# Optimization experiments

Measured on AMD Instinct MI355X. Metric: run time of the kernel, lower is better.

The kernel has to match this reference:

```python
import jax, jax.numpy as jnp
import numpy as np

B, D, HGT, WID = 32, 512, 8, 32   # batch, channels, feature map H, W
T = HGT * WID                     # 256 spatial tokens
NH, L, MAXLEN = 8, 2, 25          # heads, encoder layers, max text len


def _ln(x, s, b, eps=1e-5):
    m = jnp.mean(x, -1, keepdims=True)
    v = jnp.mean((x - m) ** 2, -1, keepdims=True)
    return (x - m) * jax.lax.rsqrt(v + eps) * s + b


def setup_inputs() -> dict:
    key = jax.random.key(0)
    ks = jax.random.split(key, 16)
    w = lambda k, shp: jax.random.normal(k, shp, jnp.float32) * 0.02
    return {
        "x": jax.random.normal(ks[0], (B, D, HGT, WID), jnp.float32),
        "encoder_word_pos": jnp.arange(T, dtype=jnp.int32),
        "gsrm_word_pos": jnp.arange(MAXLEN, dtype=jnp.int32),
        # encoder positional table
        "pos_table": w(ks[1], (T, D)),
        # per-layer encoder params (stacked over L)
        "ln1_s": jnp.ones((L, D), jnp.float32), "ln1_b": jnp.zeros((L, D), jnp.float32),
        "Wq": w(ks[2], (L, D, D)), "bq": jnp.zeros((L, D), jnp.float32),
        "Wk": w(ks[3], (L, D, D)), "bk": jnp.zeros((L, D), jnp.float32),
        "Wv": w(ks[4], (L, D, D)), "bv": jnp.zeros((L, D), jnp.float32),
        "Wo": w(ks[5], (L, D, D)), "bo": jnp.zeros((L, D), jnp.float32),
        "ln2_s": jnp.ones((L, D), jnp.float32), "ln2_b": jnp.zeros((L, D), jnp.float32),
        "W1": w(ks[6], (L, D, D)), "b1": jnp.zeros((L, D), jnp.float32),  # d_inner_hid = hidden_dim
        "W2": w(ks[7], (L, D, D)), "b2": jnp.zeros((L, D), jnp.float32),
        "lnf_s": jnp.ones((D,), jnp.float32), "lnf_b": jnp.zeros((D,), jnp.float32),
        # PVAM head params
        "fc0_w": w(ks[8], (D, D)), "fc0_b": jnp.zeros((D,), jnp.float32),
        "emb_table": w(ks[9], (MAXLEN, D)),
        "fc1_w": w(ks[10], (D,)),
    }


def _pvam(x, encoder_word_pos, gsrm_word_pos, pos_table,
          ln1_s, ln1_b, Wq, bq, Wk, bk, Wv, bv, Wo, bo,
          ln2_s, ln2_b, W1, b1, W2, b2, lnf_s, lnf_b,
          fc0_w, fc0_b, emb_table, fc1_w):
    b, c, h, wd = x.shape
    feat = x.reshape(b, c, h * wd).transpose(0, 2, 1)          # [b, t, c]
    # prepare encoder: scale + learned positional embedding (eval mode: no dropout)
    enc = feat * jnp.sqrt(jnp.float32(c)) + pos_table[encoder_word_pos]
    dk = c // NH
    scale = 1.0 / jnp.sqrt(jnp.float32(dk))
    for l in range(L):  # pre-norm transformer encoder (preprocess='n', postprocess='da')
        qin = _ln(enc, ln1_s[l], ln1_b[l])
        q = (qin @ Wq[l] + bq[l]).reshape(b, -1, NH, dk)
        k = (qin @ Wk[l] + bk[l]).reshape(b, -1, NH, dk)
        v = (qin @ Wv[l] + bv[l]).reshape(b, -1, NH, dk)
        p = jax.nn.softmax(jnp.einsum('bqhd,bkhd->bhqk', q, k) * scale, -1)
        o = jnp.einsum('bhqk,bkhd->bqhd', p, v).reshape(b, -1, c)
        enc = enc + (o @ Wo[l] + bo[l])
        y = _ln(enc, ln2_s[l], ln2_b[l])
        enc = enc + (jax.nn.relu(y @ W1[l] + b1[l]) @ W2[l] + b2[l])
    enc = _ln(enc, lnf_s, lnf_b)
    word_features = enc @ fc0_w + fc0_b                        # [b, t, c]
    word_pos = emb_table[gsrm_word_pos]                        # [max_len, c]
    # additive attention: tanh(broadcast add) -> scalar score -> softmax over t
    y = jnp.tanh(word_features[:, None, :, :] + word_pos[None, :, None, :])  # [b,max_len,t,c]
    attn = jax.nn.softmax(jnp.einsum('bmtc,c->bmt', y, fc1_w), -1)
    return jnp.einsum('bmt,btc->bmc', attn, word_features)    # [b, max_len, c]


def reference(x, encoder_word_pos, gsrm_word_pos, pos_table,
              ln1_s, ln1_b, Wq, bq, Wk, bk, Wv, bv, Wo, bo,
              ln2_s, ln2_b, W1, b1, W2, b2, lnf_s, lnf_b,
              fc0_w, fc0_b, emb_table, fc1_w):
    return _pvam(x, encoder_word_pos, gsrm_word_pos, pos_table,
                 ln1_s, ln1_b, Wq, bq, Wk, bk, Wv, bv, Wo, bo,
                 ln2_s, ln2_b, W1, b1, W2, b2, lnf_s, lnf_b,
                 fc0_w, fc0_b, emb_table, fc1_w)
```

## Files before the change

### kernel.cpp

```cpp
#include <hip/hip_runtime.h>
#include <math.h>

#define B_ 32
#define D_ 512
#define T_ 256
#define NH_ 8
#define DK_ 64
#define ML_ 25

typedef unsigned short ushort_t;
using short8 = __attribute__((ext_vector_type(8))) short;
using f32x4  = __attribute__((ext_vector_type(4))) float;

__device__ __forceinline__ ushort_t f2bf(float f) {
    unsigned u = __float_as_uint(f);
    unsigned r = (u + 0x7fffu + ((u >> 16) & 1u)) >> 16;
    return (ushort_t)r;
}
__device__ __forceinline__ float bf2f(ushort_t h) {
    return __uint_as_float(((unsigned)h) << 16);
}
__device__ __forceinline__ void gl16(const void* g, void* l) {
    __builtin_amdgcn_global_load_lds((const __attribute__((address_space(1))) void*)g,
                                     (__attribute__((address_space(3))) void*)l, 16, 0, 0);
}
#define ZERO4(v) { (v)[0]=0.f; (v)[1]=0.f; (v)[2]=0.f; (v)[3]=0.f; }

__global__ __launch_bounds__(256) void prep_kernel(const float* __restrict__ x,
                                                   const int* __restrict__ epos,
                                                   const float* __restrict__ pos,
                                                   float* __restrict__ enc) {
    __shared__ float ld[64][65];
    int tt = blockIdx.x, ct = blockIdx.y, b = blockIdx.z;
    int t0 = tt * 64, c0 = ct * 64;
    int tid = threadIdx.x;
    int r = tid >> 4, c4 = (tid & 15) << 2;
#pragma unroll
    for (int p = 0; p < 4; p++) {
        int row = p * 16 + r;
        float4 v = *(const float4*)(x + ((size_t)(b * D_ + c0 + row) * T_ + t0) + c4);
        ld[row][c4 + 0] = v.x; ld[row][c4 + 1] = v.y; ld[row][c4 + 2] = v.z; ld[row][c4 + 3] = v.w;
    }
    __syncthreads();
#pragma unroll
    for (int p = 0; p < 4; p++) {
        int tr = p * 16 + r;
        int ep = epos[t0 + tr];
        float4 pv = *(const float4*)(pos + (size_t)ep * D_ + c0 + c4);
        float4 o;
        o.x = ld[c4 + 0][tr] * 22.627417f + pv.x;
        o.y = ld[c4 + 1][tr] * 22.627417f + pv.y;
        o.z = ld[c4 + 2][tr] * 22.627417f + pv.z;
        o.w = ld[c4 + 3][tr] * 22.627417f + pv.w;
        *(float4*)(enc + (size_t)(b * T_ + t0 + tr) * D_ + c0 + c4) = o;
    }
}

__global__ __launch_bounds__(256) void convert_w_kernel(const float* __restrict__ Wq,
                                                        const float* __restrict__ Wk,
                                                        const float* __restrict__ Wv,
                                                        const float* __restrict__ Wo,
                                                        const float* __restrict__ W1,
                                                        const float* __restrict__ W2,
                                                        const float* __restrict__ fc0,
                                                        ushort_t* __restrict__ wt) {
    __shared__ float ld[64][65];
    int m = blockIdx.x >> 6;
    int tile = blockIdx.x & 63;
    int tn = tile >> 3, tk = tile & 7;
    int n0 = tn * 64, k0 = tk * 64;
    const float* src;
    if (m < 12) {
        int l = m / 6, w = m % 6;
        const float* bases[6] = {Wq, Wk, Wv, Wo, W1, W2};
        src = bases[w] + (size_t)l * D_ * D_;
    } else {
        src = fc0;
    }
    int tid = threadIdx.x;
    int r = tid >> 4, c4 = (tid & 15) << 2;
#pragma unroll
    for (int p = 0; p < 4; p++) {
        int row = p * 16 + r;
        float4 v = *(const float4*)(src + (size_t)(k0 + row) * D_ + n0 + c4);
        ld[row][c4 + 0] = v.x; ld[row][c4 + 1] = v.y; ld[row][c4 + 2] = v.z; ld[row][c4 + 3] = v.w;
    }
    __syncthreads();
    ushort_t* dsth = wt + (size_t)m * D_ * D_;
    ushort_t* dstl = wt + (size_t)13 * D_ * D_;
#pragma unroll
    for (int p = 0; p < 4; p++) {
        int n = p * 16 + r;
        int kc = c4;
        ushort_t h[4], lo[4];
#pragma unroll
        for (int i = 0; i < 4; i++) {
            float f = ld[kc + i][n];
            h[i] = f2bf(f);
            lo[i] = f2bf(f - bf2f(h[i]));
        }
        *(ushort4*)(dsth + (size_t)(n0 + n) * D_ + k0 + kc) = make_ushort4(h[0], h[1], h[2], h[3]);
        if (m == 12)
            *(ushort4*)(dstl + (size_t)(n0 + n) * D_ + k0 + kc) = make_ushort4(lo[0], lo[1], lo[2], lo[3]);
    }
}

template<bool LO>
__global__ __launch_bounds__(256) void ln_kernel(const float* __restrict__ x,
                                                 const float* __restrict__ s,
                                                 const float* __restrict__ b,
                                                 ushort_t* __restrict__ yh,
                                                 ushort_t* __restrict__ yl) {
    int wid = threadIdx.x >> 6, lane = threadIdx.x & 63;
    size_t row = (size_t)blockIdx.x * 4 + wid;
    const float4* xr = (const float4*)(x + row * D_);
    float4 v0 = xr[lane * 2], v1 = xr[lane * 2 + 1];
    float sum = v0.x + v0.y + v0.z + v0.w + v1.x + v1.y + v1.z + v1.w;
    for (int o = 32; o; o >>= 1) sum += __shfl_xor(sum, o);
    float mean = sum * (1.f / 512.f);
    float d[8] = {v0.x - mean, v0.y - mean, v0.z - mean, v0.w - mean,
                  v1.x - mean, v1.y - mean, v1.z - mean, v1.w - mean};
    float vs = 0.f;
#pragma unroll
    for (int i = 0; i < 8; i++) vs += d[i] * d[i];
    for (int o = 32; o; o >>= 1) vs += __shfl_xor(vs, o);
    float rs = 1.f / sqrtf(vs * (1.f / 512.f) + 1e-5f);
    const float4* s4 = (const float4*)s;
    const float4* b4 = (const float4*)b;
    float4 sa = s4[lane * 2], sb = s4[lane * 2 + 1];
    float4 ba = b4[lane * 2], bb = b4[lane * 2 + 1];
    float o8[8];
    o8[0] = d[0] * rs * sa.x + ba.x; o8[1] = d[1] * rs * sa.y + ba.y;
    o8[2] = d[2] * rs * sa.z + ba.z; o8[3] = d[3] * rs * sa.w + ba.w;
    o8[4] = d[4] * rs * sb.x + bb.x; o8[5] = d[5] * rs * sb.y + bb.y;
    o8[6] = d[6] * rs * sb.z + bb.z; o8[7] = d[7] * rs * sb.w + bb.w;
    ushort_t h[8];
#pragma unroll
    for (int i = 0; i < 8; i++) h[i] = f2bf(o8[i]);
    uint4 u;
    u.x = (unsigned)h[0] | ((unsigned)h[1] << 16);
    u.y = (unsigned)h[2] | ((unsigned)h[3] << 16);
    u.z = (unsigned)h[4] | ((unsigned)h[5] << 16);
    u.w = (unsigned)h[6] | ((unsigned)h[7] << 16);
    *(uint4*)(yh + row * D_ + lane * 8) = u;
    if (LO) {
        ushort_t l8[8];
#pragma unroll
        for (int i = 0; i < 8; i++) l8[i] = f2bf(o8[i] - bf2f(h[i]));
        uint4 ul;
        ul.x = (unsigned)l8[0] | ((unsigned)l8[1] << 16);
        ul.y = (unsigned)l8[2] | ((unsigned)l8[3] << 16);
        ul.z = (unsigned)l8[4] | ((unsigned)l8[5] << 16);
        ul.w = (unsigned)l8[6] | ((unsigned)l8[7] << 16);
        *(uint4*)(yl + row * D_ + lane * 8) = ul;
    }
}

template<int EPI>
__global__ __launch_bounds__(256) void gemm_kernel(const ushort_t* __restrict__ A0,
                                                   const ushort_t* __restrict__ A1,
                                                   const ushort_t* __restrict__ A2,
                                                   const ushort_t* __restrict__ B0,
                                                   const ushort_t* __restrict__ B1,
                                                   const ushort_t* __restrict__ B2,
                                                   int nseg, int nbn,
                                                   const float* __restrict__ bias,
                                                   const float* __restrict__ res,
                                                   float* __restrict__ outF,
                                                   ushort_t* __restrict__ outB) {
    __shared__ ushort_t As[3][128 * 64];
    __shared__ ushort_t Bs[3][64 * 64];
    int tid = threadIdx.x;
    int g = blockIdx.x;
    int per = gridDim.x >> 3;
    int lin = (g & 7) * per + (g >> 3);
    int bm = lin / nbn, bn = lin % nbn;

    int lane = tid & 63;
    int wid = tid >> 6;
    int wm = wid >> 1, wn = wid & 1;
    int xr = (lane & 7) << 3;

    f32x4 acc[4][2];
#pragma unroll
    for (int i = 0; i < 4; i++)
#pragma unroll
        for (int j = 0; j < 2; j++) ZERO4(acc[i][j]);

    int nt = nseg * 8;

#define STAGE(kt, buf)                                                                  \
    {                                                                                   \
        int seg_ = (kt) >> 3;                                                           \
        int k0_ = ((kt) & 7) * 64;                                                      \
        const ushort_t* Asg = seg_ == 0 ? A0 : (seg_ == 1 ? A1 : A2);                   \
        const ushort_t* Bsg = seg_ == 0 ? B0 : (seg_ == 1 ? B1 : B2);                   \
        _Pragma("unroll")                                                               \
        for (int it = 0; it < 4; it++) {                                                \
            int uu = tid + it * 256;                                                    \
            int row_ = uu >> 3;                                                         \
            int kb_ = (((uu & 7) ^ (row_ & 7)) << 3);                                   \
            gl16(Asg + (size_t)(bm * 128 + row_) * 512 + k0_ + kb_, &As[buf][uu * 8]);  \
        }                                                                               \
        _Pragma("unroll")                                                               \
        for (int it = 0; it < 2; it++) {                                                \
            int uu = tid + it * 256;                                                    \
            int row_ = uu >> 3;                                                         \
            int kb_ = (((uu & 7) ^ (row_ & 7)) << 3);                                   \
            gl16(Bsg + (size_t)(bn * 64 + row_) * 512 + k0_ + kb_, &Bs[buf][uu * 8]);   \
        }                                                                               \
    }

#define COMPUTE(bufc)                                                                        \
    {                                                                                        \
        _Pragma("unroll")                                                                    \
        for (int kc = 0; kc < 2; kc++) {                                                     \
            short8 a[4], b[2];                                                               \
            int koff = (kc * 32 + ((lane >> 4) << 3)) ^ xr;                                  \
            _Pragma("unroll")                                                                \
            for (int i = 0; i < 4; i++)                                                      \
                a[i] = *(const short8*)&As[bufc][(wm * 64 + i * 16 + (lane & 15)) * 64 + koff]; \
            _Pragma("unroll")                                                                \
            for (int j = 0; j < 2; j++)                                                      \
                b[j] = *(const short8*)&Bs[bufc][(wn * 32 + j * 16 + (lane & 15)) * 64 + koff]; \
            _Pragma("unroll")                                                                \
            for (int i = 0; i < 4; i++)                                                      \
                _Pragma("unroll")                                                            \
                for (int j = 0; j < 2; j++)                                                  \
                    acc[i][j] = __builtin_amdgcn_mfma_f32_16x16x32_bf16(a[i], b[j], acc[i][j], 0, 0, 0); \
        }                                                                                    \
    }

    STAGE(0, 0);
    if (nt > 1) STAGE(1, 1);
    asm volatile("s_waitcnt vmcnt(6)" ::: "memory");
    __builtin_amdgcn_s_barrier();

    int cur = 0;
    for (int t = 0; t < nt; t++) {
        if (t + 2 < nt) STAGE(t + 2, (cur + 2 >= 3 ? cur - 1 : cur + 2));
        COMPUTE(cur);
        if (t + 2 < nt) {
            asm volatile("s_waitcnt vmcnt(6)" ::: "memory");
        } else if (t + 1 < nt) {
            asm volatile("s_waitcnt vmcnt(0)" ::: "memory");
        }
        __builtin_amdgcn_s_barrier();
        cur = (cur == 2) ? 0 : cur + 1;
    }
#undef STAGE
#undef COMPUTE

#pragma unroll
    for (int i = 0; i < 4; i++) {
#pragma unroll
        for (int j = 0; j < 2; j++) {
            int r0 = bm * 128 + wm * 64 + i * 16 + ((lane >> 4) << 2);
            int col = bn * 64 + wn * 32 + j * 16 + (lane & 15);
            float bc = bias[col];
#pragma unroll
            for (int jj = 0; jj < 4; jj++) {
                float v = acc[i][j][jj] + bc;
                int row = r0 + jj;
                size_t idx = (size_t)row * 512 + col;
                if (EPI == 2) {
                    outF[idx] = v + res[idx];
                } else if (EPI == 3) {
                    outB[idx] = f2bf(fmaxf(v, 0.f));
                } else {
                    outF[idx] = v;
                }
            }
        }
    }
}

__global__ __launch_bounds__(256) void gemm_qkv_kernel(const ushort_t* __restrict__ A,
                                                       const ushort_t* __restrict__ W,
                                                       const float* __restrict__ bq,
                                                       const float* __restrict__ bk,
                                                       const float* __restrict__ bv,
                                                       ushort_t* __restrict__ outB) {
    __shared__ ushort_t As[2][128 * 64];
    __shared__ ushort_t Bs[2][128 * 64];
    int tid = threadIdx.x;
    int g = blockIdx.x;
    int per = gridDim.x >> 3;
    int lin = (g & 7) * per + (g >> 3);
    int bm = lin / 12, bn = lin % 12;

    int lane = tid & 63;
    int wid = tid >> 6;
    int wm = wid >> 1, wn = wid & 1;
    int xr = (lane & 7) << 3;

    f32x4 acc[4][4];
#pragma unroll
    for (int i = 0; i < 4; i++)
#pragma unroll
        for (int j = 0; j < 4; j++) ZERO4(acc[i][j]);

#define QSTAGE(kt, buf)                                                                 \
    {                                                                                   \
        int k0_ = (kt) * 64;                                                            \
        _Pragma("unroll")                                                               \
        for (int it = 0; it < 4; it++) {                                                \
            int uu = tid + it * 256;                                                    \
            int row_ = uu >> 3;                                                         \
            int kb_ = (((uu & 7) ^ (row_ & 7)) << 3);                                   \
            gl16(A + (size_t)(bm * 128 + row_) * 512 + k0_ + kb_, &As[buf][uu * 8]);    \
            gl16(W + (size_t)(bn * 128 + row_) * 512 + k0_ + kb_, &Bs[buf][uu * 8]);    \
        }                                                                               \
    }

    QSTAGE(0, 0);
    asm volatile("s_waitcnt vmcnt(0)" ::: "memory");
    __builtin_amdgcn_s_barrier();

    int buf = 0;
    for (int t = 0; t < 8; t++) {
        if (t + 1 < 8) QSTAGE(t + 1, buf ^ 1);
#pragma unroll
        for (int kc = 0; kc < 2; kc++) {
            short8 a[4], b[4];
            int koff = (kc * 32 + ((lane >> 4) << 3)) ^ xr;
#pragma unroll
            for (int i = 0; i < 4; i++)
                a[i] = *(const short8*)&As[buf][(wm * 64 + i * 16 + (lane & 15)) * 64 + koff];
#pragma unroll
            for (int j = 0; j < 4; j++)
                b[j] = *(const short8*)&Bs[buf][(wn * 64 + j * 16 + (lane & 15)) * 64 + koff];
#pragma unroll
            for (int i = 0; i < 4; i++)
#pragma unroll
                for (int j = 0; j < 4; j++)
                    acc[i][j] = __builtin_amdgcn_mfma_f32_16x16x32_bf16(a[i], b[j], acc[i][j], 0, 0, 0);
        }
        if (t + 1 < 8) asm volatile("s_waitcnt vmcnt(0)" ::: "memory");
        __builtin_amdgcn_s_barrier();
        buf ^= 1;
    }
#undef QSTAGE

#pragma unroll
    for (int i = 0; i < 4; i++) {
#pragma unroll
        for (int j = 0; j < 4; j++) {
            int r0 = bm * 128 + wm * 64 + i * 16 + ((lane >> 4) << 2);
            int col = bn * 128 + wn * 64 + j * 16 + (lane & 15);
            int seg = col >> 9;
            int ccol = col & 511;
            const float* bp = (seg == 0) ? bq : (seg == 1 ? bk : bv);
            float bc = bp[ccol];
#pragma unroll
            for (int jj = 0; jj < 4; jj++) {
                float v = acc[i][j][jj] + bc;
                int row = r0 + jj;
                if (seg < 2) {
                    outB[(size_t)seg * 4194304 + (size_t)row * 512 + ccol] = f2bf(v);
                } else {
                    int bb2 = row >> 8, t2 = row & 255;
                    outB[(size_t)2 * 4194304 +
                         ((size_t)(bb2 * 8 + (ccol >> 6)) * 64 + (ccol & 63)) * 256 + t2] = f2bf(v);
                }
            }
        }
    }
}

__global__ __launch_bounds__(256) void attn_fused_kernel(const ushort_t* __restrict__ q,
                                                         const ushort_t* __restrict__ k,
                                                         const ushort_t* __restrict__ vt,
                                                         ushort_t* __restrict__ ao) {
    __shared__ ushort_t KVs[256 * 64];
    __shared__ ushort_t Ps[64 * 256];
    int tid = threadIdx.x;
    int lane = tid & 63;
    int wid = tid >> 6;
    int m0 = blockIdx.x * 64;
    int bh = blockIdx.y;
    int b = bh >> 3, h = bh & 7;
    int xr = (lane & 7) << 3;

#pragma unroll
    for (int it = 0; it < 8; it++) {
        int uu = tid + it * 256;
        int row = uu >> 3;
        int gx = ((uu & 7) ^ (row & 7)) << 3;
        gl16(k + (size_t)(b * T_ + row) * D_ + h * DK_ + gx, &KVs[uu * 8]);
    }
    short8 qa0, qa1;
    {
        int qrow = m0 + wid * 16 + (lane & 15);
        const ushort_t* qp = q + (size_t)(b * T_ + qrow) * D_ + h * DK_ + ((lane >> 4) << 3);
        qa0 = *(const short8*)(qp);
        qa1 = *(const short8*)(qp + 32);
    }
    f32x4 acc[16];
#pragma unroll
    for (int j = 0; j < 16; j++) ZERO4(acc[j]);
    asm volatile("s_waitcnt vmcnt(0)" ::: "memory");
    __syncthreads();

#pragma unroll
    for (int j = 0; j < 16; j++) {
        int krow = j * 16 + (lane & 15);
        short8 b0 = *(const short8*)&KVs[krow * 64 + ((((lane >> 4) << 3)) ^ xr)];
        short8 b1 = *(const short8*)&KVs[krow * 64 + ((32 + ((lane >> 4) << 3)) ^ xr)];
        acc[j] = __builtin_amdgcn_mfma_f32_16x16x32_bf16(qa0, b0, acc[j], 0, 0, 0);
        acc[j] = __builtin_amdgcn_mfma_f32_16x16x32_bf16(qa1, b1, acc[j], 0, 0, 0);
    }
    __syncthreads();

#pragma unroll
    for (int it = 0; it < 8; it++) {
        int uu = tid + it * 256;
        int row = uu >> 5;
        int gx = ((uu & 31) ^ (row & 7)) << 3;
        gl16(vt + ((size_t)bh * DK_ + row) * T_ + gx, &KVs[uu * 8]);
    }

    const float C = 0.125f * 1.44269504f;
#pragma unroll
    for (int jj = 0; jj < 4; jj++) {
        float mx = -1e30f;
#pragma unroll
        for (int j = 0; j < 16; j++) mx = fmaxf(mx, acc[j][jj]);
#pragma unroll
        for (int msk = 1; msk < 16; msk <<= 1) mx = fmaxf(mx, __shfl_xor(mx, msk));
        float sm = 0.f;
#pragma unroll
        for (int j = 0; j < 16; j++) {
            float e = __builtin_amdgcn_exp2f((acc[j][jj] - mx) * C);
            acc[j][jj] = e;
            sm += e;
        }
#pragma unroll
        for (int msk = 1; msk < 16; msk <<= 1) sm += __shfl_xor(sm, msk);
        float inv = 1.f / sm;
#pragma unroll
        for (int j = 0; j < 16; j++) acc[j][jj] *= inv;
    }
#pragma unroll
    for (int j = 0; j < 16; j++) {
#pragma unroll
        for (int jj = 0; jj < 4; jj++) {
            int row = wid * 16 + ((lane >> 4) << 2) + jj;
            int col = j * 16 + (lane & 15);
            Ps[row * 256 + (col ^ ((row & 7) << 3))] = f2bf(acc[j][jj]);
        }
    }
    asm volatile("s_waitcnt vmcnt(0)" ::: "memory");
    __syncthreads();

    int wm = wid >> 1, wn = wid & 1;
    f32x4 acc2[2][2];
#pragma unroll
    for (int i = 0; i < 2; i++)
#pragma unroll
        for (int j = 0; j < 2; j++) ZERO4(acc2[i][j]);
#pragma unroll
    for (int kc = 0; kc < 8; kc++) {
        int off = (kc * 32 + ((lane >> 4) << 3)) ^ xr;
        short8 a0 = *(const short8*)&Ps[(wm * 32 + (lane & 15)) * 256 + off];
        short8 a1 = *(const short8*)&Ps[(wm * 32 + 16 + (lane & 15)) * 256 + off];
        short8 b0 = *(const short8*)&KVs[(wn * 32 + (lane & 15)) * 256 + off];
        short8 b1 = *(const short8*)&KVs[(wn * 32 + 16 + (lane & 15)) * 256 + off];
        acc2[0][0] = __builtin_amdgcn_mfma_f32_16x16x32_bf16(a0, b0, acc2[0][0], 0, 0, 0);
        acc2[0][1] = __builtin_amdgcn_mfma_f32_16x16x32_bf16(a0, b1, acc2[0][1], 0, 0, 0);
        acc2[1][0] = __builtin_amdgcn_mfma_f32_16x16x32_bf16(a1, b0, acc2[1][0], 0, 0, 0);
        acc2[1][1] = __builtin_amdgcn_mfma_f32_16x16x32_bf16(a1, b1, acc2[1][1], 0, 0, 0);
    }
#pragma unroll
    for (int i = 0; i < 2; i++)
#pragma unroll
        for (int j = 0; j < 2; j++)
#pragma unroll
            for (int jj = 0; jj < 4; jj++)
                ao[(size_t)(b * T_ + m0 + wm * 32 + i * 16 + ((lane >> 4) << 2) + jj) * D_ +
                   h * DK_ + wn * 32 + j * 16 + (lane & 15)] = f2bf(acc2[i][j][jj]);
}

__global__ __launch_bounds__(256) void scores_kernel(const float* __restrict__ wf,
                                                     const int* __restrict__ gpos,
                                                     const float* __restrict__ emb,
                                                     const float* __restrict__ w1,
                                                     float* __restrict__ scores) {
    __shared__ float wpL[5][512];
    __shared__ float w1m2[512];
    const float K2 = 2.885390082f;
    int tid = threadIdx.x;
    int b = blockIdx.y;
    int mg = blockIdx.z * 5;
    int t = blockIdx.x * 32 + (tid >> 3);
    int cg = tid & 7;
    for (int idx = tid; idx < 5 * 128; idx += 256) {
        int m = idx >> 7, w4 = idx & 127;
        float4 v = *(const float4*)(emb + (size_t)gpos[mg + m] * D_ + (w4 << 2));
        v.x *= K2; v.y *= K2; v.z *= K2; v.w *= K2;
        *(float4*)&wpL[m][w4 << 2] = v;
    }
    if (tid < 128) {
        float4 v = *(const float4*)(w1 + (tid << 2));
        v.x *= -2.f; v.y *= -2.f; v.z *= -2.f; v.w *= -2.f;
        *(float4*)&w1m2[tid << 2] = v;
    }
    float4 wfs[16];
    float W1S = 0.f;
    const float* wfr = wf + (size_t)(b * T_ + t) * D_ + (cg << 2);
#pragma unroll
    for (int j = 0; j < 16; j++) {
        float4 v = *(const float4*)(wfr + (j << 5));
        wfs[j].x = v.x * K2; wfs[j].y = v.y * K2; wfs[j].z = v.z * K2; wfs[j].w = v.w * K2;
        float4 wv = *(const float4*)(w1 + (cg << 2) + (j << 5));
        W1S += wv.x + wv.y + wv.z + wv.w;
    }
    __syncthreads();
    float s[5] = {W1S, W1S, W1S, W1S, W1S};
#pragma unroll
    for (int j = 0; j < 16; j++) {
        float4 w14 = *(const float4*)&w1m2[(cg << 2) + (j << 5)];
#pragma unroll
        for (int m = 0; m < 5; m++) {
            float4 wp4 = *(const float4*)&wpL[m][(cg << 2) + (j << 5)];
            s[m] += w14.x * __builtin_amdgcn_rcpf(__builtin_amdgcn_exp2f(wfs[j].x + wp4.x) + 1.f);
            s[m] += w14.y * __builtin_amdgcn_rcpf(__builtin_amdgcn_exp2f(wfs[j].y + wp4.y) + 1.f);
            s[m] += w14.z * __builtin_amdgcn_rcpf(__builtin_amdgcn_exp2f(wfs[j].z + wp4.z) + 1.f);
            s[m] += w14.w * __builtin_amdgcn_rcpf(__builtin_amdgcn_exp2f(wfs[j].w + wp4.w) + 1.f);
        }
    }
#pragma unroll
    for (int m = 0; m < 5; m++) {
        s[m] += __shfl_xor(s[m], 1);
        s[m] += __shfl_xor(s[m], 2);
        s[m] += __shfl_xor(s[m], 4);
    }
    if (cg == 0) {
#pragma unroll
        for (int m = 0; m < 5; m++)
            scores[((size_t)b * ML_ + mg + m) * T_ + t] = s[m];
    }
}

__global__ __launch_bounds__(256) void wsum_kernel(const float* __restrict__ scores,
                                                   const float* __restrict__ wf,
                                                   float* __restrict__ out) {
    __shared__ float at[T_][8];
    __shared__ float redmax[4][8];
    __shared__ float redsum[4][8];
    int tid = threadIdx.x;
    int lane = tid & 63, wv = tid >> 6;
    int b = blockIdx.y, m0 = blockIdx.x * 5;
    float s[5];
#pragma unroll
    for (int q = 0; q < 5; q++)
        s[q] = scores[((size_t)b * ML_ + m0 + q) * T_ + tid];
#pragma unroll
    for (int q = 0; q < 5; q++) {
        float mx = s[q];
        for (int o = 32; o; o >>= 1) mx = fmaxf(mx, __shfl_xor(mx, o));
        if (lane == 0) redmax[wv][q] = mx;
    }
    __syncthreads();
    float e[5];
#pragma unroll
    for (int q = 0; q < 5; q++) {
        float m = fmaxf(fmaxf(redmax[0][q], redmax[1][q]), fmaxf(redmax[2][q], redmax[3][q]));
        e[q] = __expf(s[q] - m);
        float sm = e[q];
        for (int o = 32; o; o >>= 1) sm += __shfl_xor(sm, o);
        if (lane == 0) redsum[wv][q] = sm;
    }
    __syncthreads();
#pragma unroll
    for (int q = 0; q < 5; q++) {
        float sm = redsum[0][q] + redsum[1][q] + redsum[2][q] + redsum[3][q];
        at[tid][q] = e[q] / sm;
    }
    __syncthreads();
    int c0 = tid << 1;
    const float* wfb = wf + (size_t)b * T_ * D_ + c0;
    float acc[5][2] = {};
    for (int t = 0; t < T_; t++) {
        float2 v = *(const float2*)(wfb + (size_t)t * D_);
        float4 a4 = *(const float4*)&at[t][0];
        float a5 = at[t][4];
        acc[0][0] += a4.x * v.x; acc[0][1] += a4.x * v.y;
        acc[1][0] += a4.y * v.x; acc[1][1] += a4.y * v.y;
        acc[2][0] += a4.z * v.x; acc[2][1] += a4.z * v.y;
        acc[3][0] += a4.w * v.x; acc[3][1] += a4.w * v.y;
        acc[4][0] += a5 * v.x;   acc[4][1] += a5 * v.y;
    }
#pragma unroll
    for (int q = 0; q < 5; q++) {
        float2 o;
        o.x = acc[q][0]; o.y = acc[q][1];
        *(float2*)(out + ((size_t)b * ML_ + m0 + q) * D_ + c0) = o;
    }
}

extern "C" void kernel_launch(void* const* d_in, const int* in_sizes, int n_in,
                              void* d_out, int out_size, void* d_ws, size_t ws_size,
                              hipStream_t stream) {
    (void)in_sizes; (void)n_in; (void)out_size; (void)ws_size;
    const float* x        = (const float*)d_in[0];
    const int*   epos     = (const int*)d_in[1];
    const int*   gpos     = (const int*)d_in[2];
    const float* pos_tab  = (const float*)d_in[3];
    const float* ln1_s    = (const float*)d_in[4];
    const float* ln1_b    = (const float*)d_in[5];
    const float* Wq       = (const float*)d_in[6];
    const float* bq       = (const float*)d_in[7];
    const float* Wk       = (const float*)d_in[8];
    const float* bk       = (const float*)d_in[9];
    const float* Wv       = (const float*)d_in[10];
    const float* bv       = (const float*)d_in[11];
    const float* Wo       = (const float*)d_in[12];
    const float* bo       = (const float*)d_in[13];
    const float* ln2_s    = (const float*)d_in[14];
    const float* ln2_b    = (const float*)d_in[15];
    const float* W1       = (const float*)d_in[16];
    const float* b1       = (const float*)d_in[17];
    const float* W2       = (const float*)d_in[18];
    const float* b2       = (const float*)d_in[19];
    const float* lnf_s    = (const float*)d_in[20];
    const float* lnf_b    = (const float*)d_in[21];
    const float* fc0_w    = (const float*)d_in[22];
    const float* fc0_b    = (const float*)d_in[23];
    const float* emb      = (const float*)d_in[24];
    const float* fc1_w    = (const float*)d_in[25];

    char* ws = (char*)d_ws;
    float*    enc = (float*)(ws);
    ushort_t* hi  = (ushort_t*)(ws + 16777216);
    ushort_t* qb  = (ushort_t*)(ws + 25165824);
    ushort_t* kb  = (ushort_t*)(ws + 33554432);
    ushort_t* lo  = (ushort_t*)(ws + 33554432);
    float*    scb = (float*)(ws + 33554432);
    ushort_t* vt  = (ushort_t*)(ws + 41943040);
    ushort_t* h1  = (ushort_t*)(ws + 41943040);
    ushort_t* ao  = (ushort_t*)(ws + 50331648);
    float*    wf  = (float*)(ws + 58720256);
    ushort_t* wt  = (ushort_t*)(ws + 75497472);
    const size_t WSL = (size_t)D_ * D_;

    convert_w_kernel<<<13 * 64, 256, 0, stream>>>(Wq, Wk, Wv, Wo, W1, W2, fc0_w, wt);
    prep_kernel<<<dim3(4, 8, 32), 256, 0, stream>>>(x, epos, pos_tab, enc);

    for (int l = 0; l < 2; l++) {
        size_t o1 = (size_t)l * D_;
        const ushort_t* WqkvT = wt + (l * 6 + 0) * WSL;
        const ushort_t* WoT = wt + (l * 6 + 3) * WSL;
        const ushort_t* W1T = wt + (l * 6 + 4) * WSL;
        const ushort_t* W2T = wt + (l * 6 + 5) * WSL;

        ln_kernel<false><<<2048, 256, 0, stream>>>(enc, ln1_s + o1, ln1_b + o1, hi, nullptr);
        gemm_qkv_kernel<<<768, 256, 0, stream>>>(hi, WqkvT, bq + o1, bk + o1, bv + o1, qb);
        attn_fused_kernel<<<dim3(4, 256), 256, 0, stream>>>(qb, kb, vt, ao);
        gemm_kernel<2><<<512, 256, 0, stream>>>(ao, nullptr, nullptr, WoT, nullptr, nullptr,
                                                1, 8, bo + o1, enc, enc, nullptr);
        ln_kernel<false><<<2048, 256, 0, stream>>>(enc, ln2_s + o1, ln2_b + o1, hi, nullptr);
        gemm_kernel<3><<<512, 256, 0, stream>>>(hi, nullptr, nullptr, W1T, nullptr, nullptr,
                                                1, 8, b1 + o1, nullptr, nullptr, h1);
        gemm_kernel<2><<<512, 256, 0, stream>>>(h1, nullptr, nullptr, W2T, nullptr, nullptr,
                                                1, 8, b2 + o1, enc, enc, nullptr);
    }

    ln_kernel<true><<<2048, 256, 0, stream>>>(enc, lnf_s, lnf_b, hi, lo);
    gemm_kernel<4><<<512, 256, 0, stream>>>(hi, lo, hi, wt + 12 * WSL, wt + 12 * WSL, wt + 13 * WSL,
                                            3, 8, fc0_b, nullptr, wf, nullptr);
    scores_kernel<<<dim3(8, 32, 5), 256, 0, stream>>>(wf, gpos, emb, fc1_w, scb);
    wsum_kernel<<<dim3(5, 32), 256, 0, stream>>>(scb, wf, (float*)d_out);
}
```

Before: 295.0 us.

## Fold LayerNorm into GEMM epilogues via row stats and precomputed weight sums

Removes the standalone LayerNorm kernels. Producers (prep and residual GEMMs) now emit bf16 copies of the raw residual and atomically accumulate per-row sum and sum-of-squares. The LN scale is folded into the weights, and per-column u=sum(s*W) and v=sum(b*W) are precomputed, so consumer GEMMs apply mean/rstd normalization in their epilogue. It also drops the third split segment of the final fc0 GEMM. The risks are E[x^2]-mu^2 variance cancellation, precision loss from running the GEMM on unnormalized bf16 activations, and extra atomics plus zero/uv kernels.

```diff
diff --git a/kernel.cpp b/kernel.cpp
--- a/kernel.cpp
+++ b/kernel.cpp
@@ -26,10 +26,62 @@
 }
 #define ZERO4(v) { (v)[0]=0.f; (v)[1]=0.f; (v)[2]=0.f; (v)[3]=0.f; }
 
+#define STATS_F (5 * 8192 * 2)
+#define UV_F    4608
+
+__global__ __launch_bounds__(256) void zero_kernel(float* __restrict__ z) {
+    int idx = blockIdx.x * 256 + threadIdx.x;
+    if (idx < (STATS_F + 2 * UV_F + 3) / 4) {
+        float4 zz = {0.f, 0.f, 0.f, 0.f};
+        ((float4*)z)[idx] = zz;
+    }
+}
+
+__global__ __launch_bounds__(256) void uv_kernel(const float* __restrict__ Wq,
+                                                 const float* __restrict__ Wk,
+                                                 const float* __restrict__ Wv,
+                                                 const float* __restrict__ W1,
+                                                 const float* __restrict__ fc0,
+                                                 const float* __restrict__ ln1_s, const float* __restrict__ ln1_b,
+                                                 const float* __restrict__ ln2_s, const float* __restrict__ ln2_b,
+                                                 const float* __restrict__ lnf_s, const float* __restrict__ lnf_b,
+                                                 float* __restrict__ u, float* __restrict__ v) {
+    int idx = blockIdx.x;
+    int k0 = blockIdx.y * 128;
+    const float* W; const float* s; const float* b; int off;
+    if (idx < 6) {
+        int l = idx / 3, w = idx % 3;
+        W = (w == 0 ? Wq : (w == 1 ? Wk : Wv)) + (size_t)l * D_ * D_;
+        s = ln1_s + l * D_; b = ln1_b + l * D_;
+        off = l * 1536 + w * 512;
+    } else if (idx < 8) {
+        int l = idx - 6;
+        W = W1 + (size_t)l * D_ * D_;
+        s = ln2_s + l * D_; b = ln2_b + l * D_;
+        off = 3072 + l * 512;
+    } else {
+        W = fc0; s = lnf_s; b = lnf_b; off = 4096;
+    }
+    int tid = threadIdx.x;
+#pragma unroll
+    for (int pass = 0; pass < 2; pass++) {
+        int c = tid + pass * 256;
+        float ua = 0.f, va = 0.f;
+        for (int k = k0; k < k0 + 128; k++) {
+            float w = W[(size_t)k * D_ + c];
+            ua += s[k] * w; va += b[k] * w;
+        }
+        atomicAdd(&u[off + c], ua);
+        atomicAdd(&v[off + c], va);
+    }
+}
+
 __global__ __launch_bounds__(256) void prep_kernel(const float* __restrict__ x,
                                                    const int* __restrict__ epos,
                                                    const float* __restrict__ pos,
-                                                   float* __restrict__ enc) {
+                                                   float* __restrict__ enc,
+                                                   ushort_t* __restrict__ hi,
+                                                   float* __restrict__ st) {
     __shared__ float ld[64][65];
     int tt = blockIdx.x, ct = blockIdx.y, b = blockIdx.z;
     int t0 = tt * 64, c0 = ct * 64;
@@ -52,7 +104,19 @@
         o.y = ld[c4 + 1][tr] * 22.627417f + pv.y;
         o.z = ld[c4 + 2][tr] * 22.627417f + pv.z;
         o.w = ld[c4 + 3][tr] * 22.627417f + pv.w;
-        *(float4*)(enc + (size_t)(b * T_ + t0 + tr) * D_ + c0 + c4) = o;
+        size_t row = (size_t)(b * T_ + t0 + tr);
+        *(float4*)(enc + row * D_ + c0 + c4) = o;
+        *(ushort4*)(hi + row * D_ + c0 + c4) = make_ushort4(f2bf(o.x), f2bf(o.y), f2bf(o.z), f2bf(o.w));
+        float sx = o.x + o.y + o.z + o.w;
+        float sq = o.x*o.x + o.y*o.y + o.z*o.z + o.w*o.w;
+        sx += __shfl_xor(sx, 1); sq += __shfl_xor(sq, 1);
+        sx += __shfl_xor(sx, 2); sq += __shfl_xor(sq, 2);
+        sx += __shfl_xor(sx, 4); sq += __shfl_xor(sq, 4);
+        sx += __shfl_xor(sx, 8); sq += __shfl_xor(sq, 8);
+        if ((tid & 15) == 0) {
+            atomicAdd(&st[2 * row], sx);
+            atomicAdd(&st[2 * row + 1], sq);
+        }
     }
 }
 
@@ -63,6 +127,9 @@
                                                         const float* __restrict__ W1,
                                                         const float* __restrict__ W2,
                                                         const float* __restrict__ fc0,
+                                                        const float* __restrict__ ln1_s,
+                                                        const float* __restrict__ ln2_s,
+                                                        const float* __restrict__ lnf_s,
                                                         ushort_t* __restrict__ wt) {
     __shared__ float ld[64][65];
     int m = blockIdx.x >> 6;
@@ -70,12 +137,16 @@
     int tn = tile >> 3, tk = tile & 7;
     int n0 = tn * 64, k0 = tk * 64;
     const float* src;
+    const float* sArr = nullptr;
     if (m < 12) {
         int l = m / 6, w = m % 6;
         const float* bases[6] = {Wq, Wk, Wv, Wo, W1, W2};
         src = bases[w] + (size_t)l * D_ * D_;
+        if (w < 3) sArr = ln1_s + l * D_;
+        else if (w == 4) sArr = ln2_s + l * D_;
     } else {
         src = fc0;
+        sArr = lnf_s;
     }
     int tid = threadIdx.x;
     int r = tid >> 4, c4 = (tid & 15) << 2;
@@ -85,6 +156,9 @@
         float4 v = *(const float4*)(src + (size_t)(k0 + row) * D_ + n0 + c4);
         ld[row][c4 + 0] = v.x; ld[row][c4 + 1] = v.y; ld[row][c4 + 2] = v.z; ld[row][c4 + 3] = v.w;
     }
+    float sv[4];
+#pragma unroll
+    for (int i = 0; i < 4; i++) sv[i] = sArr ? sArr[k0 + c4 + i] : 1.f;
     __syncthreads();
     ushort_t* dsth = wt + (size_t)m * D_ * D_;
     ushort_t* dstl = wt + (size_t)13 * D_ * D_;
@@ -95,7 +169,7 @@
         ushort_t h[4], lo[4];
 #pragma unroll
         for (int i = 0; i < 4; i++) {
-            float f = ld[kc + i][n];
+            float f = ld[kc + i][n] * sv[i];
             h[i] = f2bf(f);
             lo[i] = f2bf(f - bf2f(h[i]));
         }
@@ -105,69 +179,21 @@
     }
 }
 
-template<bool LO>
-__global__ __launch_bounds__(256) void ln_kernel(const float* __restrict__ x,
-                                                 const float* __restrict__ s,
-                                                 const float* __restrict__ b,
-                                                 ushort_t* __restrict__ yh,
-                                                 ushort_t* __restrict__ yl) {
-    int wid = threadIdx.x >> 6, lane = threadIdx.x & 63;
-    size_t row = (size_t)blockIdx.x * 4 + wid;
-    const float4* xr = (const float4*)(x + row * D_);
-    float4 v0 = xr[lane * 2], v1 = xr[lane * 2 + 1];
-    float sum = v0.x + v0.y + v0.z + v0.w + v1.x + v1.y + v1.z + v1.w;
-    for (int o = 32; o; o >>= 1) sum += __shfl_xor(sum, o);
-    float mean = sum * (1.f / 512.f);
-    float d[8] = {v0.x - mean, v0.y - mean, v0.z - mean, v0.w - mean,
-                  v1.x - mean, v1.y - mean, v1.z - mean, v1.w - mean};
-    float vs = 0.f;
-#pragma unroll
-    for (int i = 0; i < 8; i++) vs += d[i] * d[i];
-    for (int o = 32; o; o >>= 1) vs += __shfl_xor(vs, o);
-    float rs = 1.f / sqrtf(vs * (1.f / 512.f) + 1e-5f);
-    const float4* s4 = (const float4*)s;
-    const float4* b4 = (const float4*)b;
-    float4 sa = s4[lane * 2], sb = s4[lane * 2 + 1];
-    float4 ba = b4[lane * 2], bb = b4[lane * 2 + 1];
-    float o8[8];
-    o8[0] = d[0] * rs * sa.x + ba.x; o8[1] = d[1] * rs * sa.y + ba.y;
-    o8[2] = d[2] * rs * sa.z + ba.z; o8[3] = d[3] * rs * sa.w + ba.w;
-    o8[4] = d[4] * rs * sb.x + bb.x; o8[5] = d[5] * rs * sb.y + bb.y;
-    o8[6] = d[6] * rs * sb.z + bb.z; o8[7] = d[7] * rs * sb.w + bb.w;
-    ushort_t h[8];
-#pragma unroll
-    for (int i = 0; i < 8; i++) h[i] = f2bf(o8[i]);
-    uint4 u;
-    u.x = (unsigned)h[0] | ((unsigned)h[1] << 16);
-    u.y = (unsigned)h[2] | ((unsigned)h[3] << 16);
-    u.z = (unsigned)h[4] | ((unsigned)h[5] << 16);
-    u.w = (unsigned)h[6] | ((unsigned)h[7] << 16);
-    *(uint4*)(yh + row * D_ + lane * 8) = u;
-    if (LO) {
-        ushort_t l8[8];
-#pragma unroll
-        for (int i = 0; i < 8; i++) l8[i] = f2bf(o8[i] - bf2f(h[i]));
-        uint4 ul;
-        ul.x = (unsigned)l8[0] | ((unsigned)l8[1] << 16);
-        ul.y = (unsigned)l8[2] | ((unsigned)l8[3] << 16);
-        ul.z = (unsigned)l8[4] | ((unsigned)l8[5] << 16);
-        ul.w = (unsigned)l8[6] | ((unsigned)l8[7] << 16);
-        *(uint4*)(yl + row * D_ + lane * 8) = ul;
-    }
-}
-
 template<int EPI>
 __global__ __launch_bounds__(256) void gemm_kernel(const ushort_t* __restrict__ A0,
                                                    const ushort_t* __restrict__ A1,
-                                                   const ushort_t* __restrict__ A2,
                                                    const ushort_t* __restrict__ B0,
                                                    const ushort_t* __restrict__ B1,
-                                                   const ushort_t* __restrict__ B2,
                                                    int nseg, int nbn,
                                                    const float* __restrict__ bias,
                                                    const float* __restrict__ res,
                                                    float* __restrict__ outF,
-                                                   ushort_t* __restrict__ outB) {
+                                                   ushort_t* __restrict__ outB,
+                                                   ushort_t* __restrict__ outB2,
+                                                   const float* __restrict__ stIn,
+                                                   const float* __restrict__ u,
+                                                   const float* __restrict__ v,
+                                                   float* __restrict__ stOut) {
     __shared__ ushort_t As[3][128 * 64];
     __shared__ ushort_t Bs[3][64 * 64];
     int tid = threadIdx.x;
@@ -193,8 +219,8 @@
     {                                                                                   \
         int seg_ = (kt) >> 3;                                                           \
         int k0_ = ((kt) & 7) * 64;                                                      \
-        const ushort_t* Asg = seg_ == 0 ? A0 : (seg_ == 1 ? A1 : A2);                   \
-        const ushort_t* Bsg = seg_ == 0 ? B0 : (seg_ == 1 ? B1 : B2);                   \
+        const ushort_t* Asg = seg_ == 0 ? A0 : A1;                                      \
+        const ushort_t* Bsg = seg_ == 0 ? B0 : B1;                                      \
         _Pragma("unroll")                                                               \
         for (int it = 0; it < 4; it++) {                                                \
             int uu = tid + it * 256;                                                    \
@@ -251,24 +277,53 @@
 #undef STAGE
 #undef COMPUTE
 
-#pragma unroll
-    for (int i = 0; i < 4; i++) {
-#pragma unroll
-        for (int j = 0; j < 2; j++) {
-            int r0 = bm * 128 + wm * 64 + i * 16 + ((lane >> 4) << 2);
-            int col = bn * 64 + wn * 32 + j * 16 + (lane & 15);
-            float bc = bias[col];
+    if (EPI == 2 || EPI == 6) {
+#pragma unroll
+        for (int i = 0; i < 4; i++) {
 #pragma unroll
             for (int jj = 0; jj < 4; jj++) {
-                float v = acc[i][j][jj] + bc;
-                int row = r0 + jj;
-                size_t idx = (size_t)row * 512 + col;
-                if (EPI == 2) {
-                    outF[idx] = v + res[idx];
-                } else if (EPI == 3) {
-                    outB[idx] = f2bf(fmaxf(v, 0.f));
-                } else {
-                    outF[idx] = v;
+                int row = bm * 128 + wm * 64 + i * 16 + ((lane >> 4) << 2) + jj;
+                float sx = 0.f, sq = 0.f;
+#pragma unroll
+                for (int j = 0; j < 2; j++) {
+                    int col = bn * 64 + wn * 32 + j * 16 + (lane & 15);
+                    size_t idx = (size_t)row * 512 + col;
+                    float val = acc[i][j][jj] + bias[col] + res[idx];
+                    if (EPI == 2) outF[idx] = val;
+                    ushort_t hv = f2bf(val);
+                    outB[idx] = hv;
+                    if (EPI == 6) outB2[idx] = f2bf(val - bf2f(hv));
+                    sx += val; sq += val * val;
+                }
+                sx += __shfl_xor(sx, 1); sq += __shfl_xor(sq, 1);
+                sx += __shfl_xor(sx, 2); sq += __shfl_xor(sq, 2);
+                sx += __shfl_xor(sx, 4); sq += __shfl_xor(sq, 4);
+                sx += __shfl_xor(sx, 8); sq += __shfl_xor(sq, 8);
+                if ((lane & 15) == 0) {
+                    atomicAdd(&stOut[2 * row], sx);
+                    atomicAdd(&stOut[2 * row + 1], sq);
+                }
+            }
+        }
+    } else {
+#pragma unroll
+        for (int i = 0; i < 4; i++) {
+#pragma unroll
+            for (int j = 0; j < 2; j++) {
+                int col = bn * 64 + wn * 32 + j * 16 + (lane & 15);
+                float bc = bias[col];
+                float uc = u[col];
+                float vc = v[col];
+#pragma unroll
+                for (int jj = 0; jj < 4; jj++) {
+                    int row = bm * 128 + wm * 64 + i * 16 + ((lane >> 4) << 2) + jj;
+                    float s0 = stIn[2 * row], s1 = stIn[2 * row + 1];
+                    float mu = s0 * (1.f / 512.f);
+                    float rs = rsqrtf(s1 * (1.f / 512.f) - mu * mu + 1e-5f);
+                    float val = rs * (acc[i][j][jj] - mu * uc) + vc + bc;
+                    size_t idx = (size_t)row * 512 + col;
+                    if (EPI == 3) outB[idx] = f2bf(fmaxf(val, 0.f));
+                    else outF[idx] = val;
                 }
             }
         }
@@ -280,6 +335,9 @@
                                                        const float* __restrict__ bq,
                                                        const float* __restrict__ bk,
                                                        const float* __restrict__ bv,
+                                                       const float* __restrict__ stIn,
+                                                       const float* __restrict__ u,
+                                                       const float* __restrict__ v,
                                                        ushort_t* __restrict__ outB) {
     __shared__ ushort_t As[2][128 * 64];
     __shared__ ushort_t Bs[2][128 * 64];
@@ -352,16 +410,21 @@
             int ccol = col & 511;
             const float* bp = (seg == 0) ? bq : (seg == 1 ? bk : bv);
             float bc = bp[ccol];
+            float uc = u[col];
+            float vc = v[col];
 #pragma unroll
             for (int jj = 0; jj < 4; jj++) {
-                float v = acc[i][j][jj] + bc;
                 int row = r0 + jj;
+                float s0 = stIn[2 * row], s1 = stIn[2 * row + 1];
+                float mu = s0 * (1.f / 512.f);
+                float rs = rsqrtf(s1 * (1.f / 512.f) - mu * mu + 1e-5f);
+                float val = rs * (acc[i][j][jj] - mu * uc) + vc + bc;
                 if (seg < 2) {
-                    outB[(size_t)seg * 4194304 + (size_t)row * 512 + ccol] = f2bf(v);
+                    outB[(size_t)seg * 4194304 + (size_t)row * 512 + ccol] = f2bf(val);
                 } else {
                     int bb2 = row >> 8, t2 = row & 255;
                     outB[(size_t)2 * 4194304 +
-                         ((size_t)(bb2 * 8 + (ccol >> 6)) * 64 + (ccol & 63)) * 256 + t2] = f2bf(v);
+                         ((size_t)(bb2 * 8 + (ccol >> 6)) * 64 + (ccol & 63)) * 256 + t2] = f2bf(val);
                 }
             }
         }
@@ -642,10 +705,18 @@
     ushort_t* ao  = (ushort_t*)(ws + 50331648);
     float*    wf  = (float*)(ws + 58720256);
     ushort_t* wt  = (ushort_t*)(ws + 75497472);
+    float*    stats = (float*)(ws + 75497472 + 14 * 524288);
+    float*    uArr  = stats + STATS_F;
+    float*    vArr  = uArr + UV_F;
     const size_t WSL = (size_t)D_ * D_;
 
-    convert_w_kernel<<<13 * 64, 256, 0, stream>>>(Wq, Wk, Wv, Wo, W1, W2, fc0_w, wt);
-    prep_kernel<<<dim3(4, 8, 32), 256, 0, stream>>>(x, epos, pos_tab, enc);
+    zero_kernel<<<89, 256, 0, stream>>>(stats);
+    convert_w_kernel<<<13 * 64, 256, 0, stream>>>(Wq, Wk, Wv, Wo, W1, W2, fc0_w,
+                                                  ln1_s, ln2_s, lnf_s, wt);
+    uv_kernel<<<dim3(9, 4), 256, 0, stream>>>(Wq, Wk, Wv, W1, fc0_w,
+                                              ln1_s, ln1_b, ln2_s, ln2_b, lnf_s, lnf_b,
+                                              uArr, vArr);
+    prep_kernel<<<dim3(4, 8, 32), 256, 0, stream>>>(x, epos, pos_tab, enc, hi, stats);
 
     for (int l = 0; l < 2; l++) {
         size_t o1 = (size_t)l * D_;
@@ -653,22 +724,32 @@
         const ushort_t* WoT = wt + (l * 6 + 3) * WSL;
         const ushort_t* W1T = wt + (l * 6 + 4) * WSL;
         const ushort_t* W2T = wt + (l * 6 + 5) * WSL;
-
-        ln_kernel<false><<<2048, 256, 0, stream>>>(enc, ln1_s + o1, ln1_b + o1, hi, nullptr);
-        gemm_qkv_kernel<<<768, 256, 0, stream>>>(hi, WqkvT, bq + o1, bk + o1, bv + o1, qb);
+        float* stQKV = stats + (l == 0 ? 0 : 2) * 8192 * 2;
+        float* stWo  = stats + (l == 0 ? 1 : 3) * 8192 * 2;
+        float* stW2  = stats + (l == 0 ? 2 : 4) * 8192 * 2;
+
+        gemm_qkv_kernel<<<768, 256, 0, stream>>>(hi, WqkvT, bq + o1, bk + o1, bv + o1,
+                                                 stQKV, uArr + l * 1536, vArr + l * 1536, qb);
         attn_fused_kernel<<<dim3(4, 256), 256, 0, stream>>>(qb, kb, vt, ao);
-        gemm_kernel<2><<<512, 256, 0, stream>>>(ao, nullptr, nullptr, WoT, nullptr, nullptr,
-                                                1, 8, bo + o1, enc, enc, nullptr);
-        ln_kernel<false><<<2048, 256, 0, stream>>>(enc, ln2_s + o1, ln2_b + o1, hi, nullptr);
-        gemm_kernel<3><<<512, 256, 0, stream>>>(hi, nullptr, nullptr, W1T, nullptr, nullptr,
-                                                1, 8, b1 + o1, nullptr, nullptr, h1);
-        gemm_kernel<2><<<512, 256, 0, stream>>>(h1, nullptr, nullptr, W2T, nullptr, nullptr,
-                                                1, 8, b2 + o1, enc, enc, nullptr);
-    }
-
-    ln_kernel<true><<<2048, 256, 0, stream>>>(enc, lnf_s, lnf_b, hi, lo);
-    gemm_kernel<4><<<512, 256, 0, stream>>>(hi, lo, hi, wt + 12 * WSL, wt + 12 * WSL, wt + 13 * WSL,
-                                            3, 8, fc0_b, nullptr, wf, nullptr);
+        gemm_kernel<2><<<512, 256, 0, stream>>>(ao, nullptr, WoT, nullptr, 1, 8,
+                                                bo + o1, enc, enc, hi, nullptr,
+                                                nullptr, nullptr, nullptr, stWo);
+        gemm_kernel<3><<<512, 256, 0, stream>>>(hi, nullptr, W1T, nullptr, 1, 8,
+                                                b1 + o1, nullptr, nullptr, h1, nullptr,
+                                                stWo, uArr + 3072 + l * 512, vArr + 3072 + l * 512, nullptr);
+        if (l == 0)
+            gemm_kernel<2><<<512, 256, 0, stream>>>(h1, nullptr, W2T, nullptr, 1, 8,
+                                                    b2 + o1, enc, enc, hi, nullptr,
+                                                    nullptr, nullptr, nullptr, stW2);
+        else
+            gemm_kernel<6><<<512, 256, 0, stream>>>(h1, nullptr, W2T, nullptr, 1, 8,
+                                                    b2 + o1, enc, nullptr, hi, lo,
+                                                    nullptr, nullptr, nullptr, stW2);
+    }
+
+    gemm_kernel<4><<<512, 256, 0, stream>>>(hi, lo, wt + 12 * WSL, wt + 12 * WSL, 2, 8,
+                                            fc0_b, nullptr, wf, nullptr, nullptr,
+                                            stats + 4 * 8192 * 2, uArr + 4096, vArr + 4096, nullptr);
     scores_kernel<<<dim3(8, 32, 5), 256, 0, stream>>>(wf, gpos, emb, fc1_w, scb);
     wsum_kernel<<<dim3(5, 32), 256, 0, stream>>>(scb, wf, (float*)d_out);
 }
```

New measurement: 325.4 us. +10.3%, slower.
